# Performance work log

Hardware: AMD Instinct MI355X
Metric: run time of the kernel (lower is better)

The kernel has to match this reference:

```python
import jax, jax.numpy as jnp
import numpy as np

NEG = -1e9
N_HEADS = 8

def layer_norm(x, scale, bias, eps=1e-7):
    m = x.mean(-1, keepdims=True)
    v = jnp.var(x, axis=-1, keepdims=True)
    return (x - m) * jax.lax.rsqrt(v + eps) * scale + bias

def attention(x, wqkv, wo, mask):
    B, S, H = x.shape
    dh = H // N_HEADS
    q, k, v = jnp.split(x @ wqkv, 3, axis=-1)
    hsplit = lambda t: t.reshape(B, S, N_HEADS, dh).transpose(0, 2, 1, 3)
    q, k, v = hsplit(q), hsplit(k), hsplit(v)
    scores = jnp.einsum('bhqd,bhkd->bhqk', q, k) / jnp.sqrt(jnp.float32(dh))
    probs = jax.nn.softmax(scores + mask, axis=-1)
    out = jnp.einsum('bhqk,bhkd->bhqd', probs, v).transpose(0, 2, 1, 3).reshape(B, S, H)
    return out @ wo

def encoder(x, mask, wqkv, wo, ln1, w1, w2, ln2):
    for l in range(wqkv.shape[0]):  # small fixed layer count
        x = layer_norm(x + attention(x, wqkv[l], wo[l], mask), ln1[l, 0], ln1[l, 1])
        h = jax.nn.gelu(x @ w1[l]) @ w2[l]
        x = layer_norm(x + h, ln2[l, 0], ln2[l, 1])
    return x

def setup_inputs() -> dict:
    key = jax.random.key(0)
    B, C, T, H, F, L, V = 2, 16, 64, 512, 2048, 2, 32000
    ks = iter(jax.random.split(key, 64))
    nrm = lambda shape, s=0.02: jax.random.normal(next(ks), shape, jnp.float32) * s
    lnp = lambda: jnp.stack([jnp.ones(H, jnp.float32), jnp.zeros(H, jnp.float32)])
    lnL = lambda: jnp.broadcast_to(jnp.stack([jnp.ones(H, jnp.float32), jnp.zeros(H, jnp.float32)]), (L, 2, H)) + 0.0
    num_tokens = jax.random.randint(next(ks), (B, C), 2, T + 1)
    num_chunks = jax.random.randint(next(ks), (B,), C // 2, C + 1)
    raw_ids = jax.random.randint(next(ks), (B, C, T), 1, V)
    token_ids = jnp.where(jnp.arange(T)[None, None, :] < num_tokens[:, :, None], raw_ids, 0)
    def tf(pfx):
        return {pfx + '_wqkv': nrm((L, H, 3 * H)), pfx + '_wo': nrm((L, H, H)), pfx + '_ln1': lnL(),
                pfx + '_w1': nrm((L, H, F)), pfx + '_w2': nrm((L, F, H)), pfx + '_ln2': lnL()}
    d = {'token_ids': token_ids, 'num_chunks': num_chunks, 'num_tokens': num_tokens,
         'tok_emb': nrm((V, H)), 'tok_emb_ln': lnp(), 'chunk_pos': nrm((C, H)), 'chunk_emb_ln': lnp(),
         'sos': nrm((H,)), 'dec_emb': nrm((V, H)), 'dec_emb_ln': lnp(),
         'cls_dense': nrm((H, H)), 'cls_ln': lnp(), 'cls_proj': nrm((H, V)), 'cls_b': jnp.zeros((V,), jnp.float32)}
    d.update(tf('tok')); d.update(tf('chk')); d.update(tf('dec'))
    return d

def reference(token_ids, num_chunks, num_tokens, tok_emb, tok_emb_ln, tok_wqkv, tok_wo, tok_ln1, tok_w1, tok_w2, tok_ln2, chunk_pos, chunk_emb_ln, chk_wqkv, chk_wo, chk_ln1, chk_w1, chk_w2, chk_ln2, sos, dec_emb, dec_emb_ln, dec_wqkv, dec_wo, dec_ln1, dec_w1, dec_w2, dec_ln2, cls_dense, cls_ln, cls_proj, cls_b):
    B, C, T = token_ids.shape
    H = sos.shape[0]
    S2 = C + T
    # --- token encoder over stacked chunks [B*C, T] ---
    ids = token_ids.reshape(B * C, T)
    tok_valid = jnp.arange(T)[None, :] < num_tokens.reshape(B * C, 1)
    tok_amask = jnp.where(tok_valid, 0.0, NEG)[:, None, None, :]
    x = layer_norm(tok_emb[ids], tok_emb_ln[0], tok_emb_ln[1])
    token_units = encoder(x, tok_amask, tok_wqkv, tok_wo, tok_ln1, tok_w1, tok_w2, tok_ln2)
    # --- chunk encoder (patched causal): CLS unit per chunk + chunk position embs ---
    chunk_embs = token_units.reshape(B, C, T, H)[:, :, 0, :] + chunk_pos[None]
    chunk_embs = layer_norm(chunk_embs, chunk_emb_ln[0], chunk_emb_ln[1])
    chunk_valid = jnp.arange(C)[None, :] < num_chunks[:, None]  # [B,C]
    chk_amask = jnp.where(jnp.tril(jnp.ones((C, C), bool))[None] & chunk_valid[:, None, :], 0.0, NEG)[:, None]
    chunk_units = encoder(chunk_embs, chk_amask, chk_wqkv, chk_wo, chk_ln1, chk_w1, chk_w2, chk_ln2)
    chunk_units_sos = jnp.concatenate([jnp.broadcast_to(sos, (B, 1, H)), chunk_units[:, :-1]], axis=1)
    # --- ragged decoder-input assembly (vectorized scatter replacing the double python loop) ---
    dec_tok_embs = layer_norm(dec_emb[token_ids], dec_emb_ln[0], dec_emb_ln[1])  # [B,C,T,H]
    p = jnp.arange(S2); c = jnp.arange(C); n = num_tokens
    cond_prefix = (p[None, None, :] <= c[None, :, None]) & chunk_valid[:, :, None]            # [B,C,S2]
    cond_tok = (p[None, None, :] > c[None, :, None]) & (p[None, None, :] <= c[None, :, None] + n[:, :, None]) & chunk_valid[:, :, None]
    prefix = chunk_units_sos[:, jnp.minimum(p, C - 1)]                                        # [B,S2,H]
    tidx = jnp.clip(p[None, :] - c[:, None] - 1, 0, T - 1)                                    # [C,S2]
    tok_part = jnp.take_along_axis(dec_tok_embs, jnp.broadcast_to(tidx[None, :, :, None], (B, C, S2, 1)), axis=2)
    dec_in = jnp.where(cond_prefix[..., None], prefix[:, None], 0.0) + jnp.where(cond_tok[..., None], tok_part, 0.0)
    # --- causal decoder over [B*C, C+T, H] ---
    dec_amask = jnp.where(jnp.tril(jnp.ones((S2, S2), bool)), 0.0, NEG)[None, None]
    units = encoder(dec_in.reshape(B * C, S2, H), dec_amask, dec_wqkv, dec_wo, dec_ln1, dec_w1, dec_w2, dec_ln2)
    units = units.reshape(B, C, S2, H)
    # --- ragged reassembly (vectorized gather replacing the double python loop) ---
    t = jnp.arange(T - 1)
    ridx = c[:, None] + 1 + t[None, :]  # [C,T-1], always < C+T
    gathered = jnp.take_along_axis(units, jnp.broadcast_to(ridx[None, :, :, None], (B, C, T - 1, 1)), axis=2)
    rmask = (t[None, None, :] < n[:, :, None] - 1) & chunk_valid[:, :, None]
    units_re = jnp.where(rmask[..., None], gathered, 0.0)
    # --- MLM head (cls): dense + gelu + LN + vocab projection ---
    y = layer_norm(jax.nn.gelu(units_re @ cls_dense), cls_ln[0], cls_ln[1])
    logits = y @ cls_proj + cls_b  # [B,C,T-1,V]
    return logits
```

## Files before the change

### kernel.cpp

```cpp
#include <hip/hip_runtime.h>
#include <hip/hip_bf16.h>


typedef __hip_bfloat16 bf16;
typedef __attribute__((ext_vector_type(8))) short short8;
typedef __attribute__((ext_vector_type(4))) float f32x4;

__device__ inline float b2f(bf16 x) { return __bfloat162float(x); }
__device__ inline bf16 f2b(float x) { return __float2bfloat16(x); }
__device__ inline short f2bs(float x) { bf16 h = __float2bfloat16(x); return *reinterpret_cast<short*>(&h); }
__device__ inline float gelu_f(float x) {
    return 0.5f * x * (1.f + tanhf(0.7978845608028654f * (x + 0.044715f * x * x * x)));
}
__device__ __forceinline__ void gload16(const void* g, void* l) {
    __builtin_amdgcn_global_load_lds(
        (const __attribute__((address_space(1))) unsigned int*)g,
        (__attribute__((address_space(3))) unsigned int*)l, 16, 0, 0);
}

#define NMAT 26
struct TAll {
    const float* src[NMAT];
    bf16* dst[NMAT];
    int K[NMAT], N[NMAT];
    int ofs[NMAT + 1];
};

__global__ __launch_bounds__(256) void k_transpose(TAll ta) {
    __shared__ float tile[32][33];
    int bid = blockIdx.x;
    int m = 0;
    while (m + 1 < NMAT && bid >= ta.ofs[m + 1]) ++m;
    int local = bid - ta.ofs[m];
    int K = ta.K[m], N = ta.N[m];
    int tilesX = N >> 5;
    int tx = local % tilesX, ty = local / tilesX;
    int k0 = ty << 5, n0 = tx << 5;
    const float* src = ta.src[m];
    bf16* dst = ta.dst[m];
    int t = threadIdx.x;
    int c = t & 31, r = t >> 5;
#pragma unroll
    for (int p = 0; p < 4; ++p)
        tile[r + p * 8][c] = src[(long)(k0 + r + p * 8) * N + n0 + c];
    __syncthreads();
#pragma unroll
    for (int p = 0; p < 4; ++p)
        dst[(long)(n0 + r + p * 8) * K + k0 + c] = __float2bfloat16(tile[c][r + p * 8]);
}

template<int BM, int BN, int ACT, int BIAS, int OUTBF, int VT = 0, int SWZ = 0, int EPIF32 = 0, int HG = 0>
__global__ __launch_bounds__(256) void k_gemm_mfma(const bf16* __restrict__ A,
        const bf16* __restrict__ Bt, const float* __restrict__ bias,
        void* __restrict__ Cc, int M, int N, int K, bf16* __restrict__ vt, int S,
        const int* __restrict__ hg_nc = nullptr, const int* __restrict__ hg_nt = nullptr,
        const bf16* __restrict__ hg_zero = nullptr) {
    constexpr int WM = BM / 2, WN = BN / 2, FM = WM / 16, FN = WN / 16;
    constexpr int L = BM / 32 + BN / 32;
    constexpr int ASZ = BM * 64, BSZ = BN * 64;
    constexpr int SB = (ASZ + BSZ) * 2 * 2;
    constexpr int EBf = EPIF32 ? BM * (BN + 4) * 4 : 0;
    constexpr int EBv = VT ? 64 * (BN + 5) * 4 : 0;
    constexpr int SMEM = SB > EBf ? (SB > EBv ? SB : EBv) : (EBf > EBv ? EBf : EBv);
    __shared__ __align__(16) char smem[SMEM];
    short* As = (short*)smem;
    short* Bs = (short*)smem + 2 * ASZ;

    int m0, n0;
    if constexpr (SWZ) {
        int MT = gridDim.x;
        int pI = blockIdx.y * MT + blockIdx.x;
        int GS = MT << 3;
        int q = pI / GS, r = pI - q * GS;
        int mt = r >> 3, nt = q * 8 + (r & 7);
        if (nt * BN >= N) return;
        m0 = mt * BM; n0 = nt * BN;
    } else {
        m0 = blockIdx.y * BM; n0 = blockIdx.x * BN;
    }
    int tid = threadIdx.x;
    int w = tid >> 6, l = tid & 63;
    int wm = w >> 1, wn = w & 1;
    int l16 = l & 15, kg = l >> 4;
    int srow = l >> 3, scol = (l & 7) * 16;

    const char* abase[BM / 32];
#pragma unroll
    for (int p = 0; p < BM / 32; ++p) {
        int r = p * 32 + w * 8 + srow;
        if constexpr (HG) {
            int row = m0 + r;
            int bc = row / 63, t = row - bc * 63;
            int c = bc & 15, b = bc >> 4;
            bool valid = (c < hg_nc[b]) && (t < hg_nt[bc] - 1);
            abase[p] = valid ? (const char*)(A + ((long)bc * 80 + c + 1 + t) * 512)
                             : (const char*)hg_zero;
        } else {
            abase[p] = (const char*)(A + (long)(m0 + r) * K);
        }
    }

    f32x4 acc[FM][FN];
#pragma unroll
    for (int i = 0; i < FM; ++i)
#pragma unroll
        for (int j = 0; j < FN; ++j) acc[i][j] = 0.f;

    auto stage = [&](int kt, int half) {
        long kof = (long)kt * 64;
#pragma unroll
        for (int p = 0; p < BM / 32; ++p) {
            int r = p * 32 + w * 8 + srow;
            gload16(abase[p] + (kof << 1) + (scol ^ ((r & 7) << 4)),
                    (char*)As + half * (ASZ * 2) + (p * 32 + w * 8) * 128);
        }
#pragma unroll
        for (int p = 0; p < BN / 32; ++p) {
            int r = p * 32 + w * 8 + srow;
            gload16((const char*)Bt + (((long)(n0 + r) * K + kof) << 1) + (scol ^ ((r & 7) << 4)),
                    (char*)Bs + half * (BSZ * 2) + (p * 32 + w * 8) * 128);
        }
    };

    int NT = K >> 6;
    stage(0, 0);
    for (int t = 0; t < NT; ++t) {
        int cur = t & 1;
        if (t + 1 < NT) {
            stage(t + 1, cur ^ 1);
            if constexpr (L == 3)      asm volatile("s_waitcnt vmcnt(3)" ::: "memory");
            else if constexpr (L == 4) asm volatile("s_waitcnt vmcnt(4)" ::: "memory");
            else if constexpr (L == 5) asm volatile("s_waitcnt vmcnt(5)" ::: "memory");
            else if constexpr (L == 6) asm volatile("s_waitcnt vmcnt(6)" ::: "memory");
            else                       asm volatile("s_waitcnt vmcnt(8)" ::: "memory");
        } else {
            asm volatile("s_waitcnt vmcnt(0)" ::: "memory");
        }
        __builtin_amdgcn_s_barrier();
        const char* Ab = (const char*)As + cur * (ASZ * 2);
        const char* Bb = (const char*)Bs + cur * (BSZ * 2);
#pragma unroll
        for (int ks = 0; ks < 2; ++ks) {
            short8 a[FM], b[FN];
#pragma unroll
            for (int i = 0; i < FM; ++i) {
                int ar = wm * WM + i * 16 + l16;
                a[i] = *reinterpret_cast<const short8*>(Ab + ar * 128 + ((ks * 64 + kg * 16) ^ ((ar & 7) << 4)));
            }
#pragma unroll
            for (int j = 0; j < FN; ++j) {
                int br = wn * WN + j * 16 + l16;
                b[j] = *reinterpret_cast<const short8*>(Bb + br * 128 + ((ks * 64 + kg * 16) ^ ((br & 7) << 4)));
            }
#pragma unroll
            for (int i = 0; i < FM; ++i)
#pragma unroll
                for (int j = 0; j < FN; ++j)
                    acc[i][j] = __builtin_amdgcn_mfma_f32_16x16x32_bf16(a[i], b[j], acc[i][j], 0, 0, 0);
        }
        asm volatile("s_waitcnt lgkmcnt(0)" ::: "memory");
        __builtin_amdgcn_sched_barrier(0);
        __builtin_amdgcn_s_barrier();
    }

    if constexpr (EPIF32) {
        static_assert(BN == 128, "EPIF32 assumes BN=128");
        float* T = (float*)smem;
        constexpr int LDT = BN + 4;
#pragma unroll
        for (int i = 0; i < FM; ++i)
#pragma unroll
            for (int j = 0; j < FN; ++j)
#pragma unroll
                for (int jj = 0; jj < 4; ++jj)
                    T[(wm * WM + i * 16 + kg * 4 + jj) * LDT + wn * WN + j * 16 + l16] = acc[i][j][jj];
        __syncthreads();
#pragma unroll
        for (int it = 0; it < BM / 8; ++it) {
            int rr = w * (BM / 4) + it * 2 + (l >> 5);
            int row = m0 + rr;
            int col = (l & 31) * 4;
            float4 v = *reinterpret_cast<const float4*>(&T[rr * LDT + col]);
            if (BIAS) {
                float4 bb = *reinterpret_cast<const float4*>(&bias[n0 + col]);
                v.x += bb.x; v.y += bb.y; v.z += bb.z; v.w += bb.w;
            }
            if (row < M)
                *reinterpret_cast<float4*>(&((float*)Cc)[(long)row * N + n0 + col]) = v;
        }
        return;
    }
    if constexpr (VT) {
        if (n0 >= 1024) {
            float* T = (float*)smem;
            constexpr int LDV = BN + 5;
#pragma unroll
            for (int i = 0; i < FM; ++i)
#pragma unroll
                for (int j = 0; j < FN; ++j)
#pragma unroll
                    for (int jj = 0; jj < 4; ++jj)
                        T[(wm * WM + i * 16 + kg * 4 + jj) * LDV + wn * WN + j * 16 + l16] = acc[i][j][jj];
            __syncthreads();
            int SPl = ((S + 31) >> 5) << 5;
#pragma unroll
            for (int hh2 = 0; hh2 < BN / 64; ++hh2) {
                int h = ((n0 - 1024) >> 6) + hh2;
#pragma unroll
                for (int it = 0; it < 8; ++it) {
                    int d = w * 16 + it * 2 + (l >> 5);
                    int lr = (l & 31) * 2;
                    int g = m0 + lr;
                    int sq = g / S, key = g - sq * S;
                    uint pk = (uint)(unsigned short)f2bs(T[lr * LDV + hh2 * 64 + d]) |
                              ((uint)(unsigned short)f2bs(T[(lr + 1) * LDV + hh2 * 64 + d]) << 16);
                    *reinterpret_cast<uint*>(vt + (((long)(sq * 8 + h) * 64 + d) * SPl + key)) = pk;
                }
            }
            return;
        }
    }
#pragma unroll
    for (int i = 0; i < FM; ++i) {
#pragma unroll
        for (int jj = 0; jj < 4; ++jj) {
            int row = m0 + wm * WM + i * 16 + kg * 4 + jj;
            if (row < M) {
#pragma unroll
                for (int j = 0; j < FN; ++j) {
                    int col = n0 + wn * WN + j * 16 + l16;
                    float v = acc[i][j][jj];
                    if (BIAS) v += bias[col];
                    if (ACT) v = gelu_f(v);
                    if (OUTBF) ((bf16*)Cc)[(long)row * N + col] = f2b(v);
                    else       ((float*)Cc)[(long)row * N + col] = v;
                }
            }
        }
    }
}

template<int S>
__global__ __launch_bounds__(64) void k_attn_mfma(const bf16* __restrict__ qkv,
        const bf16* __restrict__ vt, bf16* __restrict__ att,
        const int* __restrict__ limits, int causal) {
    constexpr int KT = S / 16;
    constexpr int SP = ((S + 31) / 32) * 32;
    constexpr int KS = SP / 32;
    constexpr int SPAD = SP - KT * 16;
    __shared__ __align__(16) short Pw[16 * 104];
    int bid = blockIdx.x;
    int qt = bid % KT;
    int bh = bid / KT;
    int h = bh & 7, seq = bh >> 3;
    int l = threadIdx.x;
    int l16 = l & 15, kg = l >> 4;
    int lim = limits ? limits[seq] : S;
    const short* qk = (const short*)qkv + (long)seq * S * 1536 + h * 64;
    const short* vb_base = (const short*)vt + ((long)(seq * 8 + h) * 64) * SP;

    f32x4 sc[KT];
#pragma unroll
    for (int kt = 0; kt < KT; ++kt) sc[kt] = 0.f;
#pragma unroll
    for (int ks = 0; ks < 2; ++ks) {
        short8 qa = *reinterpret_cast<const short8*>(qk + (long)(qt * 16 + l16) * 1536 + ks * 32 + kg * 8);
#pragma unroll
        for (int kt = 0; kt < KT; ++kt) {
            short8 kb = *reinterpret_cast<const short8*>(qk + (long)(kt * 16 + l16) * 1536 + 512 + ks * 32 + kg * 8);
            sc[kt] = __builtin_amdgcn_mfma_f32_16x16x32_bf16(qa, kb, sc[kt], 0, 0, 0);
        }
    }
#pragma unroll
    for (int jj = 0; jj < 4; ++jj) {
        int q = qt * 16 + kg * 4 + jj;
        float vs[KT], m = -1e30f;
#pragma unroll
        for (int kt = 0; kt < KT; ++kt) {
            int key = kt * 16 + l16;
            float s = sc[kt][jj] * 0.125f;
            bool ok = (!causal || key <= q) && (key < lim);
            vs[kt] = ok ? s : -1e30f;
            m = fmaxf(m, vs[kt]);
        }
#pragma unroll
        for (int o = 1; o < 16; o <<= 1) m = fmaxf(m, __shfl_xor(m, o));
        float sum = 0.f;
#pragma unroll
        for (int kt = 0; kt < KT; ++kt) { vs[kt] = __expf(vs[kt] - m); sum += vs[kt]; }
#pragma unroll
        for (int o = 1; o < 16; o <<= 1) sum += __shfl_xor(sum, o);
        float rinv = 1.f / sum;
#pragma unroll
        for (int kt = 0; kt < KT; ++kt)
            Pw[(kg * 4 + jj) * 104 + kt * 16 + l16] = f2bs(vs[kt] * rinv);
    }
    if (SPAD > 0) {
#pragma unroll
        for (int jj = 0; jj < 4; ++jj)
            Pw[(kg * 4 + jj) * 104 + KT * 16 + l16] = 0;
    }
    f32x4 ao[4];
#pragma unroll
    for (int ct = 0; ct < 4; ++ct) ao[ct] = 0.f;
#pragma unroll
    for (int kst = 0; kst < KS; ++kst) {
        short8 pa = *reinterpret_cast<const short8*>((const char*)Pw + l16 * 208 + kst * 64 + kg * 16);
#pragma unroll
        for (int ct = 0; ct < 4; ++ct) {
            short8 vbf = *reinterpret_cast<const short8*>(vb_base + (long)(ct * 16 + l16) * SP + kst * 32 + kg * 8);
            ao[ct] = __builtin_amdgcn_mfma_f32_16x16x32_bf16(pa, vbf, ao[ct], 0, 0, 0);
        }
    }
#pragma unroll
    for (int ct = 0; ct < 4; ++ct)
#pragma unroll
        for (int jj = 0; jj < 4; ++jj) {
            int q = qt * 16 + kg * 4 + jj;
            att[((long)seq * S + q) * 512 + h * 64 + ct * 16 + l16] = f2b(ao[ct][jj]);
        }
}

__device__ inline void ln_finish(float v0, float v1, const float* __restrict__ lnw,
                                 bf16* __restrict__ outrow) {
    float s = v0 + v1, q = v0 * v0 + v1 * v1;
#pragma unroll
    for (int o = 32; o > 0; o >>= 1) { s += __shfl_xor(s, o); q += __shfl_xor(q, o); }
    __shared__ float rs[4], rq[4];
    int w = threadIdx.x >> 6;
    if ((threadIdx.x & 63) == 0) { rs[w] = s; rq[w] = q; }
    __syncthreads();
    s = rs[0] + rs[1] + rs[2] + rs[3];
    q = rq[0] + rq[1] + rq[2] + rq[3];
    float m = s * (1.f / 512.f);
    float var = q * (1.f / 512.f) - m * m;
    float inv = rsqrtf(var + 1e-7f);
    int i0 = threadIdx.x * 2, i1 = i0 + 1;
    outrow[i0] = f2b((v0 - m) * inv * lnw[i0] + lnw[512 + i0]);
    outrow[i1] = f2b((v1 - m) * inv * lnw[i1] + lnw[512 + i1]);
}

__global__ __launch_bounds__(256) void k_embed_ln2(const int* __restrict__ ids,
        const float* __restrict__ tok_emb, const float* __restrict__ tok_lnw,
        const float* __restrict__ dec_emb, const float* __restrict__ dec_lnw,
        bf16* __restrict__ x, bf16* __restrict__ dec_tok, bf16* __restrict__ zerorow) {
    int row = blockIdx.x;
    if (row >= 4096) {
        ((uint*)zerorow)[threadIdx.x] = 0u;
        return;
    }
    const float* emb; const float* lnw; bf16* out;
    if (row < 2048) { emb = tok_emb; lnw = tok_lnw; out = x + (long)row * 512; }
    else { row -= 2048; emb = dec_emb; lnw = dec_lnw; out = dec_tok + (long)row * 512; }
    const float* e = emb + (long)ids[row] * 512;
    int i0 = threadIdx.x * 2;
    ln_finish(e[i0], e[i0 + 1], lnw, out);
}

__global__ __launch_bounds__(256) void k_add_ln(const bf16* __restrict__ a, const bf16* __restrict__ b,
        const float* __restrict__ lnw, bf16* __restrict__ out) {
    int row = blockIdx.x;
    long off = (long)row * 512;
    int i0 = threadIdx.x * 2;
    float v0 = b2f(a[off + i0]), v1 = b2f(a[off + i0 + 1]);
    if (b) { v0 += b2f(b[off + i0]); v1 += b2f(b[off + i0 + 1]); }
    ln_finish(v0, v1, lnw, out + off);
}

__global__ __launch_bounds__(256) void k_chunk_ln(const bf16* __restrict__ tu, const float* __restrict__ cpos,
        const float* __restrict__ lnw, bf16* __restrict__ out) {
    int bc = blockIdx.x;
    int c = bc & 15;
    long toff = (long)bc * 64 * 512;
    int i0 = threadIdx.x * 2;
    float v0 = b2f(tu[toff + i0])     + cpos[c * 512 + i0];
    float v1 = b2f(tu[toff + i0 + 1]) + cpos[c * 512 + i0 + 1];
    ln_finish(v0, v1, lnw, out + (long)bc * 512);
}

__global__ __launch_bounds__(256) void k_dec_in(const bf16* __restrict__ chunk_units,
        const float* __restrict__ sos, const bf16* __restrict__ dec_tok,
        const int* __restrict__ num_chunks, const int* __restrict__ num_tokens,
        bf16* __restrict__ out) {
    int row = blockIdx.x;
    int p = row % 80;
    int bc = row / 80;
    int c = bc & 15, b = bc >> 4;
    int t = threadIdx.x;
    bf16* o = out + (long)row * 512;
    if (c < num_chunks[b]) {
        if (p <= c) {
            if (p == 0) {
                o[2 * t]     = f2b(sos[2 * t]);
                o[2 * t + 1] = f2b(sos[2 * t + 1]);
                return;
            }
            ((uint*)o)[t] = ((const uint*)(chunk_units + ((long)(b * 16 + p - 1)) * 512))[t];
            return;
        }
        int n = num_tokens[bc];
        if (p <= c + n) {
            ((uint*)o)[t] = ((const uint*)(dec_tok + ((long)bc * 64 + (p - c - 1)) * 512))[t];
            return;
        }
    }
    ((uint*)o)[t] = 0u;
}

template<int S>
static void run_encoder(hipStream_t st, bf16* x, int nseq, const int* limits, int causal,
                        bf16* const* wts, const float* ln1, const float* ln2,
                        bf16* qkv, bf16* vt, bf16* att, bf16* proj, bf16* x2, bf16* h1) {
    constexpr int KT = S / 16;
    int R = nseq * S;
    int gy64 = (R + 63) / 64, gy32 = (R + 31) / 32;
    for (int l = 0; l < 2; ++l) {
        k_gemm_mfma<64, 128, 0, 0, 1, 1><<<dim3(12, gy64), 256, 0, st>>>(x, wts[l * 4 + 0], nullptr, qkv, R, 1536, 512, vt, S);
        k_attn_mfma<S><<<dim3(nseq * 8 * KT), 64, 0, st>>>(qkv, vt, att, limits, causal);
        k_gemm_mfma<32, 128, 0, 0, 1><<<dim3(4, gy32), 256, 0, st>>>(att, wts[l * 4 + 1], nullptr, proj, R, 512, 512, nullptr, 0);
        k_add_ln<<<dim3(R), 256, 0, st>>>(x, proj, ln1 + (long)l * 1024, x2);
        k_gemm_mfma<64, 128, 1, 0, 1><<<dim3(16, gy64), 256, 0, st>>>(x2, wts[l * 4 + 2], nullptr, h1, R, 2048, 512, nullptr, 0);
        k_gemm_mfma<32, 128, 0, 0, 1><<<dim3(4, gy32), 256, 0, st>>>(h1, wts[l * 4 + 3], nullptr, proj, R, 512, 2048, nullptr, 0);
        k_add_ln<<<dim3(R), 256, 0, st>>>(x2, proj, ln2 + (long)l * 1024, x);
    }
}

extern "C" void kernel_launch(void* const* d_in, const int* in_sizes, int n_in,
                              void* d_out, int out_size, void* d_ws, size_t ws_size,
                              hipStream_t stream) {
    (void)in_sizes; (void)n_in; (void)out_size; (void)ws_size;
    const int*   token_ids    = (const int*)d_in[0];
    const int*   num_chunks   = (const int*)d_in[1];
    const int*   num_tokens   = (const int*)d_in[2];
    const float* tok_emb      = (const float*)d_in[3];
    const float* tok_emb_ln   = (const float*)d_in[4];
    const float* chunk_pos    = (const float*)d_in[5];
    const float* chunk_emb_ln = (const float*)d_in[6];
    const float* sos          = (const float*)d_in[7];
    const float* dec_emb      = (const float*)d_in[8];
    const float* dec_emb_ln   = (const float*)d_in[9];
    const float* cls_dense    = (const float*)d_in[10];
    const float* cls_ln       = (const float*)d_in[11];
    const float* cls_proj     = (const float*)d_in[12];
    const float* cls_b        = (const float*)d_in[13];
    const float* w_in[3][4] = {
        {(const float*)d_in[14], (const float*)d_in[15], (const float*)d_in[17], (const float*)d_in[18]},
        {(const float*)d_in[20], (const float*)d_in[21], (const float*)d_in[23], (const float*)d_in[24]},
        {(const float*)d_in[26], (const float*)d_in[27], (const float*)d_in[29], (const float*)d_in[30]},
    };
    const float* ln_in[3][2] = {
        {(const float*)d_in[16], (const float*)d_in[19]},
        {(const float*)d_in[22], (const float*)d_in[25]},
        {(const float*)d_in[28], (const float*)d_in[31]},
    };

    char* p = (char*)d_ws;
    auto carve_b = [&](size_t elems) {
        bf16* r = (bf16*)p;
        p += ((elems * 2 + 255) / 256) * 256;
        return r;
    };
    bf16* x       = carve_b((size_t)2560 * 512);
    bf16* qkv     = carve_b((size_t)2560 * 1536);
    bf16* vt      = carve_b((size_t)32 * 8 * 64 * 96);
    bf16* att     = carve_b((size_t)2560 * 512);
    bf16* proj    = carve_b((size_t)2560 * 512);
    bf16* x2      = carve_b((size_t)2560 * 512);
    bf16* h1      = carve_b((size_t)2560 * 2048);
    bf16* chunk_x = carve_b((size_t)64 * 512);
    bf16* dec_tok = carve_b((size_t)2048 * 512);
    bf16* hbuf    = carve_b((size_t)2048 * 512);
    bf16* ybuf    = carve_b((size_t)2048 * 512);
    bf16* zerorow = carve_b((size_t)512);

    TAll ta;
    int nm = 0, tiles = 0;
    auto push = [&](const float* src, int K, int N) -> bf16* {
        bf16* dst = carve_b((size_t)K * N);
        ta.src[nm] = src; ta.dst[nm] = dst; ta.K[nm] = K; ta.N[nm] = N;
        ta.ofs[nm] = tiles;
        tiles += (K / 32) * (N / 32);
        ++nm;
        return dst;
    };
    static const int KN[4][2] = {{512, 1536}, {512, 512}, {512, 2048}, {2048, 512}};
    bf16* wt[3][8];
    for (int tf = 0; tf < 3; ++tf)
        for (int l = 0; l < 2; ++l)
            for (int m = 0; m < 4; ++m) {
                int K = KN[m][0], N = KN[m][1];
                wt[tf][l * 4 + m] = push(w_in[tf][m] + (long)l * K * N, K, N);
            }
    bf16* wt_dense = push(cls_dense, 512, 512);
    bf16* wt_proj  = push(cls_proj, 512, 32000);
    ta.ofs[nm] = tiles;

    k_transpose<<<dim3(tiles), 256, 0, stream>>>(ta);

    k_embed_ln2<<<4097, 256, 0, stream>>>(token_ids, tok_emb, tok_emb_ln, dec_emb, dec_emb_ln, x, dec_tok, zerorow);

    run_encoder<64>(stream, x, 32, num_tokens, 0, wt[0], ln_in[0][0], ln_in[0][1],
                    qkv, vt, att, proj, x2, h1);
    k_chunk_ln<<<32, 256, 0, stream>>>(x, chunk_pos, chunk_emb_ln, chunk_x);
    run_encoder<16>(stream, chunk_x, 2, num_chunks, 1, wt[1], ln_in[1][0], ln_in[1][1],
                    qkv, vt, att, proj, x2, h1);
    k_dec_in<<<2560, 256, 0, stream>>>(chunk_x, sos, dec_tok, num_chunks, num_tokens, x);
    run_encoder<80>(stream, x, 32, nullptr, 1, wt[2], ln_in[2][0], ln_in[2][1],
                    qkv, vt, att, proj, x2, h1);
    k_gemm_mfma<32, 128, 1, 0, 1, 0, 0, 0, 1><<<dim3(4, 63), 256, 0, stream>>>(
        x, wt_dense, nullptr, hbuf, 2016, 512, 512, nullptr, 0,
        num_chunks, num_tokens, zerorow);
    k_add_ln<<<2016, 256, 0, stream>>>(hbuf, nullptr, cls_ln, ybuf);
    k_gemm_mfma<64, 128, 0, 1, 0, 0, 1, 1><<<dim3(32, 256), 256, 0, stream>>>(
        ybuf, wt_proj, cls_b, d_out, 2016, 32000, 512, nullptr, 0);
}
```

Baseline: 524.4 us.

## Add triple-buffered LDS pipeline for vocab GEMM and shrink encoder GEMM tiles

Generalizes the GEMM's LDS staging to a configurable depth and uses a 3-stage prefetch (two tiles in flight) for the large vocabulary projection. The encoder and dense GEMMs switch from BN=128 to BN=64 tiles, doubling the number of blocks to fill more compute units on small-M problems. The deeper pipeline raises LDS per block, which may reduce occupancy. Smaller tiles lower data reuse per block.

```diff
diff --git a/kernel.cpp b/kernel.cpp
--- a/kernel.cpp
+++ b/kernel.cpp
@@ -49,7 +49,7 @@
         dst[(long)(n0 + r + p * 8) * K + k0 + c] = __float2bfloat16(tile[c][r + p * 8]);
 }
 
-template<int BM, int BN, int ACT, int BIAS, int OUTBF, int VT = 0, int SWZ = 0, int EPIF32 = 0, int HG = 0>
+template<int BM, int BN, int ACT, int BIAS, int OUTBF, int VT = 0, int SWZ = 0, int EPIF32 = 0, int HG = 0, int DEPTH = 2>
 __global__ __launch_bounds__(256) void k_gemm_mfma(const bf16* __restrict__ A,
         const bf16* __restrict__ Bt, const float* __restrict__ bias,
         void* __restrict__ Cc, int M, int N, int K, bf16* __restrict__ vt, int S,
@@ -57,14 +57,13 @@
         const bf16* __restrict__ hg_zero = nullptr) {
     constexpr int WM = BM / 2, WN = BN / 2, FM = WM / 16, FN = WN / 16;
     constexpr int L = BM / 32 + BN / 32;
-    constexpr int ASZ = BM * 64, BSZ = BN * 64;
-    constexpr int SB = (ASZ + BSZ) * 2 * 2;
+    constexpr int ABYTES = BM * 64 * 2;
+    constexpr int STB = (BM + BN) * 64 * 2;
+    constexpr int SB = STB * DEPTH;
     constexpr int EBf = EPIF32 ? BM * (BN + 4) * 4 : 0;
     constexpr int EBv = VT ? 64 * (BN + 5) * 4 : 0;
     constexpr int SMEM = SB > EBf ? (SB > EBv ? SB : EBv) : (EBf > EBv ? EBf : EBv);
     __shared__ __align__(16) char smem[SMEM];
-    short* As = (short*)smem;
-    short* Bs = (short*)smem + 2 * ASZ;
 
     int m0, n0;
     if constexpr (SWZ) {
@@ -106,39 +105,51 @@
 #pragma unroll
         for (int j = 0; j < FN; ++j) acc[i][j] = 0.f;
 
-    auto stage = [&](int kt, int half) {
+    auto stage = [&](int kt, int s) {
         long kof = (long)kt * 64;
+        char* sb = smem + s * STB;
 #pragma unroll
         for (int p = 0; p < BM / 32; ++p) {
             int r = p * 32 + w * 8 + srow;
             gload16(abase[p] + (kof << 1) + (scol ^ ((r & 7) << 4)),
-                    (char*)As + half * (ASZ * 2) + (p * 32 + w * 8) * 128);
+                    sb + (p * 32 + w * 8) * 128);
         }
 #pragma unroll
         for (int p = 0; p < BN / 32; ++p) {
             int r = p * 32 + w * 8 + srow;
             gload16((const char*)Bt + (((long)(n0 + r) * K + kof) << 1) + (scol ^ ((r & 7) << 4)),
-                    (char*)Bs + half * (BSZ * 2) + (p * 32 + w * 8) * 128);
+                    sb + ABYTES + (p * 32 + w * 8) * 128);
         }
     };
 
     int NT = K >> 6;
     stage(0, 0);
+    if constexpr (DEPTH == 3) { if (NT > 1) stage(1, 1); }
     for (int t = 0; t < NT; ++t) {
-        int cur = t & 1;
-        if (t + 1 < NT) {
-            stage(t + 1, cur ^ 1);
-            if constexpr (L == 3)      asm volatile("s_waitcnt vmcnt(3)" ::: "memory");
-            else if constexpr (L == 4) asm volatile("s_waitcnt vmcnt(4)" ::: "memory");
-            else if constexpr (L == 5) asm volatile("s_waitcnt vmcnt(5)" ::: "memory");
-            else if constexpr (L == 6) asm volatile("s_waitcnt vmcnt(6)" ::: "memory");
-            else                       asm volatile("s_waitcnt vmcnt(8)" ::: "memory");
+        if constexpr (DEPTH == 2) {
+            if (t + 1 < NT) {
+                stage(t + 1, (t + 1) & 1);
+                if constexpr (L == 3)      asm volatile("s_waitcnt vmcnt(3)" ::: "memory");
+                else if constexpr (L == 4) asm volatile("s_waitcnt vmcnt(4)" ::: "memory");
+                else if constexpr (L == 6) asm volatile("s_waitcnt vmcnt(6)" ::: "memory");
+                else                       asm volatile("s_waitcnt vmcnt(8)" ::: "memory");
+            } else {
+                asm volatile("s_waitcnt vmcnt(0)" ::: "memory");
+            }
         } else {
-            asm volatile("s_waitcnt vmcnt(0)" ::: "memory");
+            if (t + 2 < NT) {
+                stage(t + 2, (t + 2) % 3);
+                static_assert(DEPTH != 3 || L == 6, "DEPTH3 tuned for L=6");
+                asm volatile("s_waitcnt vmcnt(12)" ::: "memory");
+            } else if (t + 1 < NT) {
+                asm volatile("s_waitcnt vmcnt(6)" ::: "memory");
+            } else {
+                asm volatile("s_waitcnt vmcnt(0)" ::: "memory");
+            }
         }
         __builtin_amdgcn_s_barrier();
-        const char* Ab = (const char*)As + cur * (ASZ * 2);
-        const char* Bb = (const char*)Bs + cur * (BSZ * 2);
+        const char* Ab = smem + (t % DEPTH) * STB;
+        const char* Bb = Ab + ABYTES;
 #pragma unroll
         for (int ks = 0; ks < 2; ++ks) {
             short8 a[FM], b[FN];
@@ -415,12 +426,12 @@
     int R = nseq * S;
     int gy64 = (R + 63) / 64, gy32 = (R + 31) / 32;
     for (int l = 0; l < 2; ++l) {
-        k_gemm_mfma<64, 128, 0, 0, 1, 1><<<dim3(12, gy64), 256, 0, st>>>(x, wts[l * 4 + 0], nullptr, qkv, R, 1536, 512, vt, S);
+        k_gemm_mfma<64, 64, 0, 0, 1, 1><<<dim3(24, gy64), 256, 0, st>>>(x, wts[l * 4 + 0], nullptr, qkv, R, 1536, 512, vt, S);
         k_attn_mfma<S><<<dim3(nseq * 8 * KT), 64, 0, st>>>(qkv, vt, att, limits, causal);
-        k_gemm_mfma<32, 128, 0, 0, 1><<<dim3(4, gy32), 256, 0, st>>>(att, wts[l * 4 + 1], nullptr, proj, R, 512, 512, nullptr, 0);
+        k_gemm_mfma<32, 64, 0, 0, 1><<<dim3(8, gy32), 256, 0, st>>>(att, wts[l * 4 + 1], nullptr, proj, R, 512, 512, nullptr, 0);
         k_add_ln<<<dim3(R), 256, 0, st>>>(x, proj, ln1 + (long)l * 1024, x2);
-        k_gemm_mfma<64, 128, 1, 0, 1><<<dim3(16, gy64), 256, 0, st>>>(x2, wts[l * 4 + 2], nullptr, h1, R, 2048, 512, nullptr, 0);
-        k_gemm_mfma<32, 128, 0, 0, 1><<<dim3(4, gy32), 256, 0, st>>>(h1, wts[l * 4 + 3], nullptr, proj, R, 512, 2048, nullptr, 0);
+        k_gemm_mfma<64, 64, 1, 0, 1><<<dim3(32, gy64), 256, 0, st>>>(x2, wts[l * 4 + 2], nullptr, h1, R, 2048, 512, nullptr, 0);
+        k_gemm_mfma<32, 64, 0, 0, 1><<<dim3(8, gy32), 256, 0, st>>>(h1, wts[l * 4 + 3], nullptr, proj, R, 512, 2048, nullptr, 0);
         k_add_ln<<<dim3(R), 256, 0, st>>>(x2, proj, ln2 + (long)l * 1024, x);
     }
 }
@@ -507,10 +518,10 @@
     k_dec_in<<<2560, 256, 0, stream>>>(chunk_x, sos, dec_tok, num_chunks, num_tokens, x);
     run_encoder<80>(stream, x, 32, nullptr, 1, wt[2], ln_in[2][0], ln_in[2][1],
                     qkv, vt, att, proj, x2, h1);
-    k_gemm_mfma<32, 128, 1, 0, 1, 0, 0, 0, 1><<<dim3(4, 63), 256, 0, stream>>>(
+    k_gemm_mfma<32, 64, 1, 0, 1, 0, 0, 0, 1><<<dim3(8, 63), 256, 0, stream>>>(
         x, wt_dense, nullptr, hbuf, 2016, 512, 512, nullptr, 0,
         num_chunks, num_tokens, zerorow);
     k_add_ln<<<2016, 256, 0, stream>>>(hbuf, nullptr, cls_ln, ybuf);
-    k_gemm_mfma<64, 128, 0, 1, 0, 0, 1, 1><<<dim3(32, 256), 256, 0, stream>>>(
+    k_gemm_mfma<64, 128, 0, 1, 0, 0, 1, 1, 0, 3><<<dim3(32, 256), 256, 0, stream>>>(
         ybuf, wt_proj, cls_b, d_out, 2016, 32000, 512, nullptr, 0);
 }
```

New measurement: 525.1 us. About the same (+0.1%).
